# Performance work log

Hardware: AMD Instinct MI355X
Metric: run time of the kernel (lower is better)

## Reference

```python
import jax, jax.numpy as jnp
import numpy as np

B, L, K, H = 512, 512, 103, 512
I = K + 2  # LSTM input = obs(103) + fed-back pos(2)


def setup_inputs() -> dict:
    key = jax.random.key(0)
    ks = jax.random.split(key, 14)
    s = 0.02
    return {
        "x": jax.random.normal(ks[0], (B, L, K), dtype=jnp.float32),
        "pos": jax.random.normal(ks[1], (B, L, 2), dtype=jnp.float32),
        "hidden_state": jnp.zeros((B, H), dtype=jnp.float32),
        "cell_state": jnp.zeros((B, H), dtype=jnp.float32),
        # LSTM params (PyTorch layout: gates ordered i,f,g,o)
        "W_ih": jax.random.normal(ks[2], (4 * H, I), dtype=jnp.float32) * s,
        "W_hh": jax.random.normal(ks[3], (4 * H, H), dtype=jnp.float32) * s,
        "b_ih": jnp.zeros((4 * H,), dtype=jnp.float32),
        "b_hh": jnp.zeros((4 * H,), dtype=jnp.float32),
        # MLP: H -> 64 -> 16 -> 2, all ReLU
        "W1": jax.random.normal(ks[4], (64, H), dtype=jnp.float32) * s,
        "b1": jnp.zeros((64,), dtype=jnp.float32),
        "W2": jax.random.normal(ks[5], (16, 64), dtype=jnp.float32) * s,
        "b2": jnp.zeros((16,), dtype=jnp.float32),
        "W3": jax.random.normal(ks[6], (2, 16), dtype=jnp.float32) * s,
        "b3": jnp.zeros((2,), dtype=jnp.float32),
    }


def reference(x, pos, hidden_state, cell_state, W_ih, W_hh, b_ih, b_hh,
              W1, b1, W2, b2, W3, b3):
    b = b_ih + b_hh

    def step(carry, x_t):
        h, c, ip = carry  # (B,H),(B,H),(B,2)
        inp = jnp.concatenate([x_t, ip], axis=-1)  # (B, I)
        gates = inp @ W_ih.T + h @ W_hh.T + b      # (B, 4H)
        i, f, g, o = jnp.split(gates, 4, axis=-1)
        c = jax.nn.sigmoid(f) * c + jax.nn.sigmoid(i) * jnp.tanh(g)
        h = jax.nn.sigmoid(o) * jnp.tanh(c)
        y = jax.nn.relu(h @ W1.T + b1)
        y = jax.nn.relu(y @ W2.T + b2)
        y = jax.nn.relu(y @ W3.T + b3)  # (B,2) predicted next pos
        return (h, c, y), y

    xs = jnp.swapaxes(x, 0, 1)  # (L,B,K)
    (h, c, _), ys = jax.lax.scan(step, (hidden_state, cell_state, pos[:, 0, :]), xs)
    predicted_pos = jnp.swapaxes(ys, 0, 1)  # (B,L,2)
    return predicted_pos, h, c
```

## Files before the change

kernel.cpp:

```cpp
#include <hip/hip_runtime.h>

#define NB 512
#define NL 512
#define NK 103
#define NH 512
#define NI 105
#define XROW (NL * NK)

typedef _Float16 half8 __attribute__((ext_vector_type(8)));
typedef _Float16 half4 __attribute__((ext_vector_type(4)));
typedef float floatx4 __attribute__((ext_vector_type(4)));

union U16 { half8 h; unsigned long long u[2]; };

#define XB_STR 136
#define B2_STR 136
#define YST_STR 72
#define Y2_STR 16
#define OFF_XB  0
#define OFF_B2  34816
#define OFF_YST 52224
#define OFF_Y2  61440
#define OFF_FR  63488
#define SMEM_BYTES 65280

#define SPIN_MAX (1 << 20)

#define A_LOAD(p)  __hip_atomic_load((p),  __ATOMIC_RELAXED, __HIP_MEMORY_SCOPE_AGENT)
#define A_STORE(p, v) __hip_atomic_store((p), (v), __ATOMIC_RELAXED, __HIP_MEMORY_SCOPE_AGENT)


__device__ __forceinline__ float fast_sigmoid(float v) {
  v = fminf(fmaxf(v, -30.f), 30.f);
  return __builtin_amdgcn_rcpf(1.f + __expf(-v));
}
__device__ __forceinline__ float fast_tanh(float v) {
  v = fminf(fmaxf(v, -15.f), 15.f);
  float e = __expf(-2.f * v);
  return (1.f - e) * __builtin_amdgcn_rcpf(1.f + e);
}

__global__ void __launch_bounds__(256, 1)
lstm_persist(const float* __restrict__ x, const float* __restrict__ pos,
             const float* __restrict__ h0, const float* __restrict__ c0,
             const float* __restrict__ Wih, const float* __restrict__ Whh,
             const float* __restrict__ bih, const float* __restrict__ bhh,
             const float* __restrict__ W1, const float* __restrict__ b1,
             const float* __restrict__ W2, const float* __restrict__ b2,
             const float* __restrict__ W3, const float* __restrict__ b3,
             float* __restrict__ out, void* __restrict__ ws)
{
  extern __shared__ char smem[];
  _Float16* B2s = (_Float16*)(smem + OFF_B2);
  _Float16* YST = (_Float16*)(smem + OFF_YST);
  _Float16* Y2  = (_Float16*)(smem + OFF_Y2);
  _Float16* HTX = Y2;
  float* FR  = (float*)(smem + OFF_FR);
  float* b1s = FR;
  float* b2s = FR + 64;
  float* w3s = FR + 80;
  float* b3s = FR + 112;
  float* wy0 = FR + 114;
  float* wy1 = FR + 178;
  float* bgs = FR + 242;
  float* ypres = FR + 306;
  volatile int* abflag = (volatile int*)(FR + 440);

  const int tid = threadIdx.x;
  const int g  = blockIdx.x >> 5;
  const int cs = blockIdx.x & 31;
  const int w  = tid >> 6, l = tid & 63;
  const int c16 = l & 15, q = l >> 4;
  const int rh = w >> 1;
  const int ch = w & 1;

  unsigned* flags = (unsigned*)ws;
  char* hbase = (char*)ws + 4096;

  if (tid == 0) *abflag = 0;
  {
    unsigned* xz = (unsigned*)(smem + OFF_XB);
    for (int i = tid; i < 8704; i += 256) xz[i] = 0;
  }
  for (int idx = tid; idx < 64 * 128; idx += 256) {
    int cc = idx >> 7, k = idx & 127;
    int gr = (cc >> 4) * NH + cs * 16 + (cc & 15);
    float v = (k < NK) ? Wih[(size_t)gr * NI + k] : 0.f;
    B2s[cc * B2_STR + k] = (_Float16)v;
  }
  if (tid < 64) {
    int gr = (tid >> 4) * NH + cs * 16 + (tid & 15);
    wy0[tid] = Wih[(size_t)gr * NI + 103];
    wy1[tid] = Wih[(size_t)gr * NI + 104];
    bgs[tid] = bih[gr] + bhh[gr];
    b1s[tid] = b1[tid];
  }
  if (tid < 16) b2s[tid] = b2[tid];
  if (tid < 32) w3s[tid] = W3[tid];
  if (tid < 2)  b3s[tid] = b3[tid];

  {
    const int r = tid >> 2, hb = tid & 3;
    const float* src = h0 + (size_t)(64 * g + r) * NH + cs * 16 + hb * 4;
    union { unsigned long long u; half4 h; } cv;
    cv.h[0] = (_Float16)src[0]; cv.h[1] = (_Float16)src[1];
    cv.h[2] = (_Float16)src[2]; cv.h[3] = (_Float16)src[3];
    A_STORE((unsigned long long*)(hbase + (size_t)cs * 16384
                                  + (size_t)(64 * g + r) * 32 + hb * 8), cv.u);
  }

  half8 bfr[4][16];
  #pragma unroll
  for (int ct = 0; ct < 4; ++ct) {
    const int rown = ch ? (ct * 16 + c16) : (ct * NH + cs * 16 + c16);
    const float* rp = (ch ? W1 : Whh) + (size_t)rown * NH;
    #pragma unroll
    for (int kk = 0; kk < 16; ++kk) {
      const float* p = rp + kk * 32 + q * 8;
      floatx4 f0 = *(const floatx4*)(p);
      floatx4 f1 = *(const floatx4*)(p + 4);
      half8 hv;
      hv[0]=(_Float16)f0[0]; hv[1]=(_Float16)f0[1]; hv[2]=(_Float16)f0[2]; hv[3]=(_Float16)f0[3];
      hv[4]=(_Float16)f1[0]; hv[5]=(_Float16)f1[1]; hv[6]=(_Float16)f1[2]; hv[7]=(_Float16)f1[3];
      bfr[ct][kk] = hv;
    }
  }
  half8 w2f[2];
  if (ch) {
    #pragma unroll
    for (int kk = 0; kk < 2; ++kk) {
      const float* p = W2 + c16 * 64 + kk * 32 + q * 8;
      floatx4 f0 = *(const floatx4*)(p);
      floatx4 f1 = *(const floatx4*)(p + 4);
      half8 hv;
      hv[0]=(_Float16)f0[0]; hv[1]=(_Float16)f0[1]; hv[2]=(_Float16)f0[2]; hv[3]=(_Float16)f0[3];
      hv[4]=(_Float16)f1[0]; hv[5]=(_Float16)f1[1]; hv[6]=(_Float16)f1[2]; hv[7]=(_Float16)f1[3];
      w2f[kk] = hv;
    }
  }
  float cacc[2][4];
  if (!ch) {
    #pragma unroll
    for (int rt = 0; rt < 2; ++rt)
      #pragma unroll
      for (int reg = 0; reg < 4; ++reg)
        cacc[rt][reg] = c0[(size_t)(64 * g + 32 * rh + 16 * rt + q * 4 + reg) * NH + cs * 16 + c16];
  }

  auto xstage = [&](int t1) {
    _Float16* xb = (_Float16*)(smem + OFF_XB) + (size_t)(t1 & 1) * 64 * XB_STR;
    const int row = 32 * rh + (l >> 1);
    const int p = l & 1;
    const float* src = x + (size_t)(64 * g + row) * XROW + (size_t)t1 * NK + p * 52;
    _Float16* dst = xb + row * XB_STR + p * 52;
    const int nfull = p ? 12 : 13;
    for (int cnk = 0; cnk < nfull; ++cnk) {
      float f0 = src[cnk * 4 + 0], f1 = src[cnk * 4 + 1];
      float f2 = src[cnk * 4 + 2], f3 = src[cnk * 4 + 3];
      half4 hv; hv[0]=(_Float16)f0; hv[1]=(_Float16)f1; hv[2]=(_Float16)f2; hv[3]=(_Float16)f3;
      *(half4*)(dst + cnk * 4) = hv;
    }
    if (p) {
      dst[48] = (_Float16)src[48];
      dst[49] = (_Float16)src[49];
      dst[50] = (_Float16)src[50];
    }
  };

  auto fpub = [&](unsigned val) {
    if (tid == 0) A_STORE(flags + ((g << 5) + cs) * 4, val);
  };

  __syncthreads();
  if (!ch) xstage(0);
  __syncthreads();
  fpub(1);

  for (int t = 0; t <= NL; ++t) {
    if (l < 32) {
      unsigned* f = flags + ((g << 5) + l) * 4;
      int spins = 0;
      while (A_LOAD(f) < (unsigned)(t + 1)) {
        if (++spins > SPIN_MAX) { *abflag = 1; break; }
      }
    }

    U16 ar[2][16];
    {
      const char* lb = hbase + (size_t)(t & 1) * 524288
                     + (size_t)(q >> 1) * 16384
                     + (size_t)(64 * g + 32 * rh + c16) * 32 + (q & 1) * 16;
      #pragma unroll
      for (int kk = 0; kk < 16; ++kk) {
        #pragma unroll
        for (int rt = 0; rt < 2; ++rt) {
          const unsigned long long* up =
              (const unsigned long long*)(lb + (size_t)kk * 32768 + rt * 512);
          ar[rt][kk].u[0] = A_LOAD(up);
          ar[rt][kk].u[1] = A_LOAD(up + 1);
        }
      }
    }

    floatx4 acc[4][2] = {};

    if (!ch && t < NL) {
      const _Float16* xb = (const _Float16*)(smem + OFF_XB) + (size_t)(t & 1) * 64 * XB_STR;
      #pragma unroll
      for (int kb = 0; kb < 4; ++kb) {
        half8 ax[2];
        #pragma unroll
        for (int rt = 0; rt < 2; ++rt)
          ax[rt] = *(const half8*)(xb + (32 * rh + 16 * rt + c16) * XB_STR + kb * 32 + q * 8);
        #pragma unroll
        for (int ct = 0; ct < 4; ++ct) {
          half8 bf = *(const half8*)(B2s + (ct * 16 + c16) * B2_STR + kb * 32 + q * 8);
          #pragma unroll
          for (int rt = 0; rt < 2; ++rt)
            acc[ct][rt] = __builtin_amdgcn_mfma_f32_16x16x32_f16(ax[rt], bf, acc[ct][rt], 0, 0, 0);
        }
      }
      if (t + 1 < NL) xstage(t + 1);
    }

    #pragma unroll
    for (int kk = 0; kk < 16; ++kk)
      #pragma unroll
      for (int ct = 0; ct < 4; ++ct) {
        acc[ct][0] = __builtin_amdgcn_mfma_f32_16x16x32_f16(ar[0][kk].h, bfr[ct][kk], acc[ct][0], 0, 0, 0);
        acc[ct][1] = __builtin_amdgcn_mfma_f32_16x16x32_f16(ar[1][kk].h, bfr[ct][kk], acc[ct][1], 0, 0, 0);
      }

    if (ch) {
      if (t == 0) {
        if (l < 32) {
          int row = 32 * rh + l;
          const float* pp = pos + (size_t)(64 * g + row) * (NL * 2);
          ypres[row * 2 + 0] = pp[0];
          ypres[row * 2 + 1] = pp[1];
        }
      } else {
        #pragma unroll
        for (int ct = 0; ct < 4; ++ct)
          #pragma unroll
          for (int rt = 0; rt < 2; ++rt)
            #pragma unroll
            for (int reg = 0; reg < 4; ++reg) {
              int row = 32 * rh + 16 * rt + q * 4 + reg;
              float v = acc[ct][rt][reg] + b1s[ct * 16 + c16];
              YST[row * YST_STR + ct * 16 + c16] = (_Float16)fmaxf(v, 0.f);
            }
        floatx4 a2c[2] = {};
        #pragma unroll
        for (int kk2 = 0; kk2 < 2; ++kk2)
          #pragma unroll
          for (int rt = 0; rt < 2; ++rt) {
            half8 af = *(const half8*)(YST + (32 * rh + 16 * rt + c16) * YST_STR + kk2 * 32 + q * 8);
            a2c[rt] = __builtin_amdgcn_mfma_f32_16x16x32_f16(af, w2f[kk2], a2c[rt], 0, 0, 0);
          }
        #pragma unroll
        for (int rt = 0; rt < 2; ++rt)
          #pragma unroll
          for (int reg = 0; reg < 4; ++reg) {
            int row = 32 * rh + 16 * rt + q * 4 + reg;
            float v = a2c[rt][reg] + b2s[c16];
            Y2[row * Y2_STR + c16] = (_Float16)fmaxf(v, 0.f);
          }
        if (l < 32) {
          int row = 32 * rh + l;
          float y0 = b3s[0], y1 = b3s[1];
          #pragma unroll
          for (int k = 0; k < 16; ++k) {
            float vv = (float)Y2[row * Y2_STR + k];
            y0 += vv * w3s[k];
            y1 += vv * w3s[16 + k];
          }
          y0 = fmaxf(y0, 0.f); y1 = fmaxf(y1, 0.f);
          ypres[row * 2 + 0] = y0;
          ypres[row * 2 + 1] = y1;
          if (cs == 0) {
            float2* op = (float2*)(out + (size_t)(64 * g + row) * (NL * 2) + (size_t)(t - 1) * 2);
            *op = make_float2(y0, y1);
          }
        }
      }
    }
    __syncthreads();
    if (*abflag) return;

    if (!ch && t < NL) {
      #pragma unroll
      for (int rt = 0; rt < 2; ++rt)
        #pragma unroll
        for (int reg = 0; reg < 4; ++reg) {
          int rl = 32 * rh + 16 * rt + q * 4 + reg;
          float yp0 = ypres[rl * 2], yp1 = ypres[rl * 2 + 1];
          float gi = acc[0][rt][reg] + bgs[c16]      + yp0 * wy0[c16]      + yp1 * wy1[c16];
          float gf = acc[1][rt][reg] + bgs[16 + c16] + yp0 * wy0[16 + c16] + yp1 * wy1[16 + c16];
          float gg = acc[2][rt][reg] + bgs[32 + c16] + yp0 * wy0[32 + c16] + yp1 * wy1[32 + c16];
          float go = acc[3][rt][reg] + bgs[48 + c16] + yp0 * wy0[48 + c16] + yp1 * wy1[48 + c16];
          float iv = fast_sigmoid(gi);
          float fv = fast_sigmoid(gf);
          float gv = fast_tanh(gg);
          float ov = fast_sigmoid(go);
          float cn = fv * cacc[rt][reg] + iv * gv;
          cacc[rt][reg] = cn;
          float hn = ov * fast_tanh(cn);
          HTX[rl * 16 + c16] = (_Float16)hn;
          if (t == NL - 1) {
            out[(size_t)(NB * NL * 2) + (size_t)(64 * g + rl) * NH + cs * 16 + c16] = hn;
            out[(size_t)(NB * NL * 2) + (size_t)(NB * NH) + (size_t)(64 * g + rl) * NH + cs * 16 + c16] = cn;
          }
        }
    }

    if (t < NL) {
      __syncthreads();
      {
        const int r = tid >> 2, hb = tid & 3;
        char* dst = hbase + (size_t)((t + 1) & 1) * 524288
                  + (size_t)cs * 16384 + (size_t)(64 * g + r) * 32 + hb * 8;
        unsigned long long v = *(const unsigned long long*)(HTX + r * 16 + hb * 4);
        A_STORE((unsigned long long*)dst, v);
      }
      __syncthreads();
      fpub((unsigned)(t + 2));
    }
  }
}

extern "C" void kernel_launch(void* const* d_in, const int* in_sizes, int n_in,
                              void* d_out, int out_size, void* d_ws, size_t ws_size,
                              hipStream_t stream) {
  (void)in_sizes; (void)n_in; (void)out_size; (void)ws_size;
  const float* x   = (const float*)d_in[0];
  const float* pos = (const float*)d_in[1];
  const float* h0  = (const float*)d_in[2];
  const float* c0  = (const float*)d_in[3];
  const float* Wih = (const float*)d_in[4];
  const float* Whh = (const float*)d_in[5];
  const float* bih = (const float*)d_in[6];
  const float* bhh = (const float*)d_in[7];
  const float* W1  = (const float*)d_in[8];
  const float* b1  = (const float*)d_in[9];
  const float* W2  = (const float*)d_in[10];
  const float* b2  = (const float*)d_in[11];
  const float* W3  = (const float*)d_in[12];
  const float* b3  = (const float*)d_in[13];
  float* out = (float*)d_out;

  hipMemsetAsync(d_ws, 0, 4096, stream);

  void* args[] = { (void*)&x, (void*)&pos, (void*)&h0, (void*)&c0,
                   (void*)&Wih, (void*)&Whh, (void*)&bih, (void*)&bhh,
                   (void*)&W1, (void*)&b1, (void*)&W2, (void*)&b2,
                   (void*)&W3, (void*)&b3, (void*)&out, (void*)&d_ws };

  hipError_t err = hipLaunchCooperativeKernel(
      reinterpret_cast<void*>(lstm_persist),
      dim3(256, 1, 1), dim3(256, 1, 1), args, (unsigned)SMEM_BYTES, stream);
  if (err != hipSuccess) {
    (void)hipGetLastError();
    lstm_persist<<<dim3(256, 1, 1), dim3(256, 1, 1), SMEM_BYTES, stream>>>(
        x, pos, h0, c0, Wih, Whh, bih, bhh, W1, b1, W2, b2, W3, b3, out, d_ws);
  }
}
```

Measured before the change: 5.382 ms.

## Stage per-group h tile into LDS with coalesced loads and remap blocks

Relayouts the global hidden-state exchange buffer so each group's 64-row h tile is contiguous and MFMA-fragment ordered. Each block loads the whole tile cooperatively with fully coalesced 16-byte loads (each wave one contiguous slice), writes it to a new 64KB LDS tile, syncs, then reads A fragments from LDS. This replaces each wave's redundant scattered atomic global loads of the full h operand. Block-to-(group,slice) mapping is interleaved so the 32 blocks of a group land on different dies/XCDs, and dynamic shared memory is raised to about 128KB, which adds an extra barrier per step and more LDS use.

```diff
diff --git a/kernel.cpp b/kernel.cpp
--- a/kernel.cpp
+++ b/kernel.cpp
@@ -10,19 +10,22 @@
 typedef _Float16 half8 __attribute__((ext_vector_type(8)));
 typedef _Float16 half4 __attribute__((ext_vector_type(4)));
 typedef float floatx4 __attribute__((ext_vector_type(4)));
-
-union U16 { half8 h; unsigned long long u[2]; };
+typedef unsigned int uint32x4 __attribute__((ext_vector_type(4)));
 
 #define XB_STR 136
 #define B2_STR 136
 #define YST_STR 72
 #define Y2_STR 16
-#define OFF_XB  0
-#define OFF_B2  34816
-#define OFF_YST 52224
-#define OFF_Y2  61440
-#define OFF_FR  63488
-#define SMEM_BYTES 65280
+#define OFF_XB   0
+#define OFF_B2   34816
+#define OFF_YST  52224
+#define OFF_Y2   61440
+#define OFF_FR   63488
+#define OFF_TILE 65280
+#define SMEM_BYTES 130816
+
+#define GBUF  524288
+#define GTILE 65536
 
 #define SPIN_MAX (1 << 20)
 
@@ -67,8 +70,8 @@
   volatile int* abflag = (volatile int*)(FR + 440);
 
   const int tid = threadIdx.x;
-  const int g  = blockIdx.x >> 5;
-  const int cs = blockIdx.x & 31;
+  const int g  = blockIdx.x & 7;
+  const int cs = blockIdx.x >> 3;
   const int w  = tid >> 6, l = tid & 63;
   const int c16 = l & 15, q = l >> 4;
   const int rh = w >> 1;
@@ -76,8 +79,10 @@
 
   unsigned* flags = (unsigned*)ws;
   char* hbase = (char*)ws + 4096;
+  char* tilebase = smem + OFF_TILE;
 
   if (tid == 0) *abflag = 0;
+
   {
     unsigned* xz = (unsigned*)(smem + OFF_XB);
     for (int i = tid; i < 8704; i += 256) xz[i] = 0;
@@ -105,8 +110,10 @@
     union { unsigned long long u; half4 h; } cv;
     cv.h[0] = (_Float16)src[0]; cv.h[1] = (_Float16)src[1];
     cv.h[2] = (_Float16)src[2]; cv.h[3] = (_Float16)src[3];
-    A_STORE((unsigned long long*)(hbase + (size_t)cs * 16384
-                                  + (size_t)(64 * g + r) * 32 + hb * 8), cv.u);
+    char* dst = hbase + (size_t)g * GTILE + (size_t)(cs >> 1) * 4096
+              + (size_t)(r >> 4) * 1024 + (size_t)(r & 15) * 64
+              + (size_t)((cs & 1) * 2 + (hb >> 1)) * 16 + (size_t)(hb & 1) * 8;
+    A_STORE((unsigned long long*)dst, cv.u);
   }
 
   half8 bfr[4][16];
@@ -167,38 +174,29 @@
     }
   };
 
-  auto fpub = [&](unsigned val) {
-    if (tid == 0) A_STORE(flags + ((g << 5) + cs) * 4, val);
-  };
-
   __syncthreads();
   if (!ch) xstage(0);
   __syncthreads();
-  fpub(1);
+  if (tid == 0) A_STORE(flags + ((g << 5) + cs) * 4, 1u);
 
   for (int t = 0; t <= NL; ++t) {
     if (l < 32) {
-      unsigned* f = flags + ((g << 5) + l) * 4;
+      const unsigned* f = flags + ((g << 5) + l) * 4;
       int spins = 0;
       while (A_LOAD(f) < (unsigned)(t + 1)) {
         if (++spins > SPIN_MAX) { *abflag = 1; break; }
       }
     }
 
-    U16 ar[2][16];
+    union { uint32x4 v; unsigned long long u[2]; } stg[16];
     {
-      const char* lb = hbase + (size_t)(t & 1) * 524288
-                     + (size_t)(q >> 1) * 16384
-                     + (size_t)(64 * g + 32 * rh + c16) * 32 + (q & 1) * 16;
-      #pragma unroll
-      for (int kk = 0; kk < 16; ++kk) {
-        #pragma unroll
-        for (int rt = 0; rt < 2; ++rt) {
-          const unsigned long long* up =
-              (const unsigned long long*)(lb + (size_t)kk * 32768 + rt * 512);
-          ar[rt][kk].u[0] = A_LOAD(up);
-          ar[rt][kk].u[1] = A_LOAD(up + 1);
-        }
+      const char* sb = hbase + (size_t)(t & 1) * GBUF + (size_t)g * GTILE
+                     + (size_t)(w * 1024) + (size_t)(l * 16);
+      #pragma unroll
+      for (int i = 0; i < 16; ++i) {
+        const unsigned long long* sp = (const unsigned long long*)(sb + i * 4096);
+        stg[i].u[0] = A_LOAD(sp);
+        stg[i].u[1] = A_LOAD(sp + 1);
       }
     }
 
@@ -223,13 +221,27 @@
       if (t + 1 < NL) xstage(t + 1);
     }
 
-    #pragma unroll
-    for (int kk = 0; kk < 16; ++kk)
-      #pragma unroll
-      for (int ct = 0; ct < 4; ++ct) {
-        acc[ct][0] = __builtin_amdgcn_mfma_f32_16x16x32_f16(ar[0][kk].h, bfr[ct][kk], acc[ct][0], 0, 0, 0);
-        acc[ct][1] = __builtin_amdgcn_mfma_f32_16x16x32_f16(ar[1][kk].h, bfr[ct][kk], acc[ct][1], 0, 0, 0);
-      }
+    {
+      char* dl = tilebase + w * 1024 + l * 16;
+      #pragma unroll
+      for (int i = 0; i < 16; ++i)
+        *(uint32x4*)(dl + i * 4096) = stg[i].v;
+    }
+    __syncthreads();
+
+    if (ch || t < NL) {
+      const char* tb = tilebase + (size_t)rh * 2048 + (size_t)c16 * 64 + (size_t)q * 16;
+      #pragma unroll
+      for (int kk = 0; kk < 16; ++kk) {
+        half8 a0 = *(const half8*)(tb + kk * 4096);
+        half8 a1 = *(const half8*)(tb + kk * 4096 + 1024);
+        #pragma unroll
+        for (int ct = 0; ct < 4; ++ct) {
+          acc[ct][0] = __builtin_amdgcn_mfma_f32_16x16x32_f16(a0, bfr[ct][kk], acc[ct][0], 0, 0, 0);
+          acc[ct][1] = __builtin_amdgcn_mfma_f32_16x16x32_f16(a1, bfr[ct][kk], acc[ct][1], 0, 0, 0);
+        }
+      }
+    }
 
     if (ch) {
       if (t == 0) {
@@ -318,13 +330,15 @@
       __syncthreads();
       {
         const int r = tid >> 2, hb = tid & 3;
-        char* dst = hbase + (size_t)((t + 1) & 1) * 524288
-                  + (size_t)cs * 16384 + (size_t)(64 * g + r) * 32 + hb * 8;
+        char* dst = hbase + (size_t)((t + 1) & 1) * GBUF + (size_t)g * GTILE
+                  + (size_t)(cs >> 1) * 4096
+                  + (size_t)(r >> 4) * 1024 + (size_t)(r & 15) * 64
+                  + (size_t)((cs & 1) * 2 + (hb >> 1)) * 16 + (size_t)(hb & 1) * 8;
         unsigned long long v = *(const unsigned long long*)(HTX + r * 16 + hb * 4);
         A_STORE((unsigned long long*)dst, v);
       }
       __syncthreads();
-      fpub((unsigned)(t + 2));
+      if (tid == 0) A_STORE(flags + ((g << 5) + cs) * 4, (unsigned)(t + 2));
     }
   }
 }
@@ -349,6 +363,13 @@
   const float* b3  = (const float*)d_in[13];
   float* out = (float*)d_out;
 
+  static bool smem_attr_set = false;
+  if (!smem_attr_set) {
+    (void)hipFuncSetAttribute(reinterpret_cast<const void*>(lstm_persist),
+                              hipFuncAttributeMaxDynamicSharedMemorySize, SMEM_BYTES);
+    smem_attr_set = true;
+  }
+
   hipMemsetAsync(d_ws, 0, 4096, stream);
 
   void* args[] = { (void*)&x, (void*)&pos, (void*)&h0, (void*)&c0,
```

Result: slower. 6.040 ms (+12.2%).

## Use per-group atomic counter barrier and contiguous per-group hidden-state tiles

Applied to the files above, without the earlier changes.

Replaces the 32 per-block flags that each block polled with a single atomic counter per batch group that all threads poll until it reaches 32*(t+1). The exchanged hidden state is re-laid out so each group's tile is one contiguous 64KB region, with 64-byte rows that make each lane's reads contiguous. Block-to-group mapping is also interleaved (g = bid&7) so groups spread across the device. It trades many flag reads for contention on one hot counter, and all 256 threads now spin instead of 32.

```diff
diff --git a/kernel.cpp b/kernel.cpp
--- a/kernel.cpp
+++ b/kernel.cpp
@@ -23,6 +23,9 @@
 #define OFF_Y2  61440
 #define OFF_FR  63488
 #define SMEM_BYTES 65280
+
+#define GBUF  524288
+#define GTILE 65536
 
 #define SPIN_MAX (1 << 20)
 
@@ -67,17 +70,18 @@
   volatile int* abflag = (volatile int*)(FR + 440);
 
   const int tid = threadIdx.x;
-  const int g  = blockIdx.x >> 5;
-  const int cs = blockIdx.x & 31;
+  const int g  = blockIdx.x & 7;
+  const int cs = blockIdx.x >> 3;
   const int w  = tid >> 6, l = tid & 63;
   const int c16 = l & 15, q = l >> 4;
   const int rh = w >> 1;
   const int ch = w & 1;
 
-  unsigned* flags = (unsigned*)ws;
+  unsigned* cnt = (unsigned*)ws + (size_t)g * 16;
   char* hbase = (char*)ws + 4096;
 
   if (tid == 0) *abflag = 0;
+
   {
     unsigned* xz = (unsigned*)(smem + OFF_XB);
     for (int i = tid; i < 8704; i += 256) xz[i] = 0;
@@ -105,8 +109,10 @@
     union { unsigned long long u; half4 h; } cv;
     cv.h[0] = (_Float16)src[0]; cv.h[1] = (_Float16)src[1];
     cv.h[2] = (_Float16)src[2]; cv.h[3] = (_Float16)src[3];
-    A_STORE((unsigned long long*)(hbase + (size_t)cs * 16384
-                                  + (size_t)(64 * g + r) * 32 + hb * 8), cv.u);
+    char* dst = hbase + (size_t)g * GTILE + (size_t)(cs >> 1) * 4096
+              + (size_t)(r >> 4) * 1024 + (size_t)(r & 15) * 64
+              + (size_t)((cs & 1) * 2 + (hb >> 1)) * 16 + (size_t)(hb & 1) * 8;
+    A_STORE((unsigned long long*)dst, cv.u);
   }
 
   half8 bfr[4][16];
@@ -167,35 +173,31 @@
     }
   };
 
-  auto fpub = [&](unsigned val) {
-    if (tid == 0) A_STORE(flags + ((g << 5) + cs) * 4, val);
-  };
-
   __syncthreads();
   if (!ch) xstage(0);
   __syncthreads();
-  fpub(1);
+  if (tid == 0)
+    __hip_atomic_fetch_add(cnt, 1u, __ATOMIC_RELAXED, __HIP_MEMORY_SCOPE_AGENT);
 
   for (int t = 0; t <= NL; ++t) {
-    if (l < 32) {
-      unsigned* f = flags + ((g << 5) + l) * 4;
+    {
+      const unsigned target = 32u * (unsigned)(t + 1);
       int spins = 0;
-      while (A_LOAD(f) < (unsigned)(t + 1)) {
+      while (A_LOAD(cnt) < target) {
         if (++spins > SPIN_MAX) { *abflag = 1; break; }
       }
     }
 
     U16 ar[2][16];
     {
-      const char* lb = hbase + (size_t)(t & 1) * 524288
-                     + (size_t)(q >> 1) * 16384
-                     + (size_t)(64 * g + 32 * rh + c16) * 32 + (q & 1) * 16;
+      const char* lb = hbase + (size_t)(t & 1) * GBUF + (size_t)g * GTILE
+                     + (size_t)(2 * rh) * 1024 + (size_t)c16 * 64 + (size_t)q * 16;
       #pragma unroll
       for (int kk = 0; kk < 16; ++kk) {
         #pragma unroll
         for (int rt = 0; rt < 2; ++rt) {
           const unsigned long long* up =
-              (const unsigned long long*)(lb + (size_t)kk * 32768 + rt * 512);
+              (const unsigned long long*)(lb + (size_t)kk * 4096 + rt * 1024);
           ar[rt][kk].u[0] = A_LOAD(up);
           ar[rt][kk].u[1] = A_LOAD(up + 1);
         }
@@ -318,13 +320,16 @@
       __syncthreads();
       {
         const int r = tid >> 2, hb = tid & 3;
-        char* dst = hbase + (size_t)((t + 1) & 1) * 524288
-                  + (size_t)cs * 16384 + (size_t)(64 * g + r) * 32 + hb * 8;
+        char* dst = hbase + (size_t)((t + 1) & 1) * GBUF + (size_t)g * GTILE
+                  + (size_t)(cs >> 1) * 4096
+                  + (size_t)(r >> 4) * 1024 + (size_t)(r & 15) * 64
+                  + (size_t)((cs & 1) * 2 + (hb >> 1)) * 16 + (size_t)(hb & 1) * 8;
         unsigned long long v = *(const unsigned long long*)(HTX + r * 16 + hb * 4);
         A_STORE((unsigned long long*)dst, v);
       }
       __syncthreads();
-      fpub((unsigned)(t + 2));
+      if (tid == 0)
+        __hip_atomic_fetch_add(cnt, 1u, __ATOMIC_RELAXED, __HIP_MEMORY_SCOPE_AGENT);
     }
   }
 }
```

New measurement: 5.458 ms. No clear change (+1.4%).

## Interleave two batch groups per block to overlap recurrent step latency

Applied to the files above, without the earlier changes.

Halves the grid to 128 blocks, and each block now handles two independent batch groups (gA and gB) for the same hidden-column slice, alternating half-steps between them. While one group waits on its cross-block flag, the other group's step can proceed, hiding synchronization latency, and the resident weight fragments are reused across both groups. The cost is double the x staging buffers and cell-state registers, a larger shared-memory footprint that needs an attribute set, and half as many CUs in use, so each block does twice the serial work.

```diff
diff --git a/kernel.cpp b/kernel.cpp
--- a/kernel.cpp
+++ b/kernel.cpp
@@ -18,12 +18,13 @@
 #define YST_STR 72
 #define Y2_STR 16
 #define OFF_XB  0
-#define OFF_B2  34816
-#define OFF_YST 52224
-#define OFF_Y2  61440
-#define OFF_FR  63488
-#define SMEM_BYTES 65280
-
+#define OFF_B2  69632
+#define OFF_YST 87040
+#define OFF_Y2  96256
+#define OFF_FR  98304
+#define SMEM_BYTES 100608
+
+#define GBUF  524288
 #define SPIN_MAX (1 << 20)
 
 #define A_LOAD(p)  __hip_atomic_load((p),  __ATOMIC_RELAXED, __HIP_MEMORY_SCOPE_AGENT)
@@ -39,6 +40,9 @@
   float e = __expf(-2.f * v);
   return (1.f - e) * __builtin_amdgcn_rcpf(1.f + e);
 }
+
+struct Tag0 { static constexpr int v = 0; };
+struct Tag1 { static constexpr int v = 1; };
 
 __global__ void __launch_bounds__(256, 1)
 lstm_persist(const float* __restrict__ x, const float* __restrict__ pos,
@@ -63,12 +67,13 @@
   float* wy0 = FR + 114;
   float* wy1 = FR + 178;
   float* bgs = FR + 242;
-  float* ypres = FR + 306;
-  volatile int* abflag = (volatile int*)(FR + 440);
+  float* ypresb = FR + 306;
+  volatile int* abflag = (volatile int*)(FR + 564);
 
   const int tid = threadIdx.x;
-  const int g  = blockIdx.x >> 5;
-  const int cs = blockIdx.x & 31;
+  const int gA = blockIdx.x & 3;
+  const int gB = gA + 4;
+  const int cs = blockIdx.x >> 2;
   const int w  = tid >> 6, l = tid & 63;
   const int c16 = l & 15, q = l >> 4;
   const int rh = w >> 1;
@@ -78,9 +83,10 @@
   char* hbase = (char*)ws + 4096;
 
   if (tid == 0) *abflag = 0;
+
   {
     unsigned* xz = (unsigned*)(smem + OFF_XB);
-    for (int i = tid; i < 8704; i += 256) xz[i] = 0;
+    for (int i = tid; i < 17408; i += 256) xz[i] = 0;
   }
   for (int idx = tid; idx < 64 * 128; idx += 256) {
     int cc = idx >> 7, k = idx & 127;
@@ -99,14 +105,16 @@
   if (tid < 32) w3s[tid] = W3[tid];
   if (tid < 2)  b3s[tid] = b3[tid];
 
-  {
+  #pragma unroll
+  for (int hh = 0; hh < 2; ++hh) {
+    const int G = hh ? gB : gA;
     const int r = tid >> 2, hb = tid & 3;
-    const float* src = h0 + (size_t)(64 * g + r) * NH + cs * 16 + hb * 4;
+    const float* src = h0 + (size_t)(64 * G + r) * NH + cs * 16 + hb * 4;
     union { unsigned long long u; half4 h; } cv;
     cv.h[0] = (_Float16)src[0]; cv.h[1] = (_Float16)src[1];
     cv.h[2] = (_Float16)src[2]; cv.h[3] = (_Float16)src[3];
     A_STORE((unsigned long long*)(hbase + (size_t)cs * 16384
-                                  + (size_t)(64 * g + r) * 32 + hb * 8), cv.u);
+                                  + (size_t)(64 * G + r) * 32 + hb * 8), cv.u);
   }
 
   half8 bfr[4][16];
@@ -138,20 +146,24 @@
       w2f[kk] = hv;
     }
   }
-  float cacc[2][4];
+  float cacc[2][2][4];
   if (!ch) {
     #pragma unroll
-    for (int rt = 0; rt < 2; ++rt)
-      #pragma unroll
-      for (int reg = 0; reg < 4; ++reg)
-        cacc[rt][reg] = c0[(size_t)(64 * g + 32 * rh + 16 * rt + q * 4 + reg) * NH + cs * 16 + c16];
-  }
-
-  auto xstage = [&](int t1) {
-    _Float16* xb = (_Float16*)(smem + OFF_XB) + (size_t)(t1 & 1) * 64 * XB_STR;
+    for (int hh = 0; hh < 2; ++hh) {
+      const int G = hh ? gB : gA;
+      #pragma unroll
+      for (int rt = 0; rt < 2; ++rt)
+        #pragma unroll
+        for (int reg = 0; reg < 4; ++reg)
+          cacc[hh][rt][reg] = c0[(size_t)(64 * G + 32 * rh + 16 * rt + q * 4 + reg) * NH + cs * 16 + c16];
+    }
+  }
+
+  auto xstage = [&](int h, int G, int t1) {
+    _Float16* xb = (_Float16*)(smem + OFF_XB) + (size_t)h * 17408 + (size_t)(t1 & 1) * 8704;
     const int row = 32 * rh + (l >> 1);
     const int p = l & 1;
-    const float* src = x + (size_t)(64 * g + row) * XROW + (size_t)t1 * NK + p * 52;
+    const float* src = x + (size_t)(64 * G + row) * XROW + (size_t)t1 * NK + p * 52;
     _Float16* dst = xb + row * XB_STR + p * 52;
     const int nfull = p ? 12 : 13;
     for (int cnk = 0; cnk < nfull; ++cnk) {
@@ -167,18 +179,20 @@
     }
   };
 
-  auto fpub = [&](unsigned val) {
-    if (tid == 0) A_STORE(flags + ((g << 5) + cs) * 4, val);
-  };
-
   __syncthreads();
-  if (!ch) xstage(0);
+  if (!ch) { xstage(0, gA, 0); xstage(1, gB, 0); }
   __syncthreads();
-  fpub(1);
-
-  for (int t = 0; t <= NL; ++t) {
+  if (tid == 0) {
+    A_STORE(flags + ((gA << 5) + cs) * 4, 1u);
+    A_STORE(flags + ((gB << 5) + cs) * 4, 1u);
+  }
+
+  auto half_step = [&](auto TG, int G, int t) -> bool {
+    constexpr int h = decltype(TG)::v;
+    float* ypres = ypresb + h * 128;
+
     if (l < 32) {
-      unsigned* f = flags + ((g << 5) + l) * 4;
+      const unsigned* f = flags + ((G << 5) + l) * 4;
       int spins = 0;
       while (A_LOAD(f) < (unsigned)(t + 1)) {
         if (++spins > SPIN_MAX) { *abflag = 1; break; }
@@ -187,9 +201,9 @@
 
     U16 ar[2][16];
     {
-      const char* lb = hbase + (size_t)(t & 1) * 524288
+      const char* lb = hbase + (size_t)(t & 1) * GBUF
                      + (size_t)(q >> 1) * 16384
-                     + (size_t)(64 * g + 32 * rh + c16) * 32 + (q & 1) * 16;
+                     + (size_t)(64 * G + 32 * rh + c16) * 32 + (q & 1) * 16;
       #pragma unroll
       for (int kk = 0; kk < 16; ++kk) {
         #pragma unroll
@@ -205,7 +219,7 @@
     floatx4 acc[4][2] = {};
 
     if (!ch && t < NL) {
-      const _Float16* xb = (const _Float16*)(smem + OFF_XB) + (size_t)(t & 1) * 64 * XB_STR;
+      const _Float16* xb = (const _Float16*)(smem + OFF_XB) + (size_t)h * 17408 + (size_t)(t & 1) * 8704;
       #pragma unroll
       for (int kb = 0; kb < 4; ++kb) {
         half8 ax[2];
@@ -220,22 +234,24 @@
             acc[ct][rt] = __builtin_amdgcn_mfma_f32_16x16x32_f16(ax[rt], bf, acc[ct][rt], 0, 0, 0);
         }
       }
-      if (t + 1 < NL) xstage(t + 1);
-    }
-
-    #pragma unroll
-    for (int kk = 0; kk < 16; ++kk)
-      #pragma unroll
-      for (int ct = 0; ct < 4; ++ct) {
-        acc[ct][0] = __builtin_amdgcn_mfma_f32_16x16x32_f16(ar[0][kk].h, bfr[ct][kk], acc[ct][0], 0, 0, 0);
-        acc[ct][1] = __builtin_amdgcn_mfma_f32_16x16x32_f16(ar[1][kk].h, bfr[ct][kk], acc[ct][1], 0, 0, 0);
-      }
+      if (t + 1 < NL) xstage(h, G, t + 1);
+    }
+
+    if (ch || t < NL) {
+      #pragma unroll
+      for (int kk = 0; kk < 16; ++kk)
+        #pragma unroll
+        for (int ct = 0; ct < 4; ++ct) {
+          acc[ct][0] = __builtin_amdgcn_mfma_f32_16x16x32_f16(ar[0][kk].h, bfr[ct][kk], acc[ct][0], 0, 0, 0);
+          acc[ct][1] = __builtin_amdgcn_mfma_f32_16x16x32_f16(ar[1][kk].h, bfr[ct][kk], acc[ct][1], 0, 0, 0);
+        }
+    }
 
     if (ch) {
       if (t == 0) {
         if (l < 32) {
           int row = 32 * rh + l;
-          const float* pp = pos + (size_t)(64 * g + row) * (NL * 2);
+          const float* pp = pos + (size_t)(64 * G + row) * (NL * 2);
           ypres[row * 2 + 0] = pp[0];
           ypres[row * 2 + 1] = pp[1];
         }
@@ -279,14 +295,14 @@
           ypres[row * 2 + 0] = y0;
           ypres[row * 2 + 1] = y1;
           if (cs == 0) {
-            float2* op = (float2*)(out + (size_t)(64 * g + row) * (NL * 2) + (size_t)(t - 1) * 2);
+            float2* op = (float2*)(out + (size_t)(64 * G + row) * (NL * 2) + (size_t)(t - 1) * 2);
             *op = make_float2(y0, y1);
           }
         }
       }
     }
     __syncthreads();
-    if (*abflag) return;
+    if (*abflag) return true;
 
     if (!ch && t < NL) {
       #pragma unroll
@@ -303,13 +319,13 @@
           float fv = fast_sigmoid(gf);
           float gv = fast_tanh(gg);
           float ov = fast_sigmoid(go);
-          float cn = fv * cacc[rt][reg] + iv * gv;
-          cacc[rt][reg] = cn;
+          float cn = fv * cacc[h][rt][reg] + iv * gv;
+          cacc[h][rt][reg] = cn;
           float hn = ov * fast_tanh(cn);
           HTX[rl * 16 + c16] = (_Float16)hn;
           if (t == NL - 1) {
-            out[(size_t)(NB * NL * 2) + (size_t)(64 * g + rl) * NH + cs * 16 + c16] = hn;
-            out[(size_t)(NB * NL * 2) + (size_t)(NB * NH) + (size_t)(64 * g + rl) * NH + cs * 16 + c16] = cn;
+            out[(size_t)(NB * NL * 2) + (size_t)(64 * G + rl) * NH + cs * 16 + c16] = hn;
+            out[(size_t)(NB * NL * 2) + (size_t)(NB * NH) + (size_t)(64 * G + rl) * NH + cs * 16 + c16] = cn;
           }
         }
     }
@@ -318,14 +334,20 @@
       __syncthreads();
       {
         const int r = tid >> 2, hb = tid & 3;
-        char* dst = hbase + (size_t)((t + 1) & 1) * 524288
-                  + (size_t)cs * 16384 + (size_t)(64 * g + r) * 32 + hb * 8;
+        char* dst = hbase + (size_t)((t + 1) & 1) * GBUF
+                  + (size_t)cs * 16384 + (size_t)(64 * G + r) * 32 + hb * 8;
         unsigned long long v = *(const unsigned long long*)(HTX + r * 16 + hb * 4);
         A_STORE((unsigned long long*)dst, v);
       }
       __syncthreads();
-      fpub((unsigned)(t + 2));
-    }
+      if (tid == 0) A_STORE(flags + ((G << 5) + cs) * 4, (unsigned)(t + 2));
+    }
+    return false;
+  };
+
+  for (int t = 0; t <= NL; ++t) {
+    if (half_step(Tag0{}, gA, t)) return;
+    if (half_step(Tag1{}, gB, t)) return;
   }
 }
 
@@ -349,6 +371,13 @@
   const float* b3  = (const float*)d_in[13];
   float* out = (float*)d_out;
 
+  static bool smem_attr_set = false;
+  if (!smem_attr_set) {
+    (void)hipFuncSetAttribute(reinterpret_cast<const void*>(lstm_persist),
+                              hipFuncAttributeMaxDynamicSharedMemorySize, SMEM_BYTES);
+    smem_attr_set = true;
+  }
+
   hipMemsetAsync(d_ws, 0, 4096, stream);
 
   void* args[] = { (void*)&x, (void*)&pos, (void*)&h0, (void*)&c0,
@@ -358,10 +387,10 @@
 
   hipError_t err = hipLaunchCooperativeKernel(
       reinterpret_cast<void*>(lstm_persist),
-      dim3(256, 1, 1), dim3(256, 1, 1), args, (unsigned)SMEM_BYTES, stream);
+      dim3(128, 1, 1), dim3(256, 1, 1), args, (unsigned)SMEM_BYTES, stream);
   if (err != hipSuccess) {
     (void)hipGetLastError();
-    lstm_persist<<<dim3(256, 1, 1), dim3(256, 1, 1), SMEM_BYTES, stream>>>(
+    lstm_persist<<<dim3(128, 1, 1), dim3(256, 1, 1), SMEM_BYTES, stream>>>(
         x, pos, h0, c0, Wih, Whh, bih, bhh, W1, b1, W2, b2, W3, b3, out, d_ws);
   }
 }
```

After: 9.280 ms. 72.4% more time.
